# Optimization experiments

Measured on AMD Instinct MI355X. Metric: run time of the kernel, lower is better.

The kernel has to match this reference:

```python
import jax, jax.numpy as jnp
import numpy as np


def setup_inputs() -> dict:
    key = jax.random.key(0)
    kx, kd = jax.random.split(key)
    B, C, T_phone = 32, 512, 1024
    x = jax.random.normal(kx, (B, C, T_phone), dtype=jnp.float32)
    durations = jax.random.randint(kd, (B, T_phone), 0, 8, dtype=jnp.int32)
    return {"x": x, "durations": durations}


def reference(x, durations):
    # x: [B, C, T_phone] float; durations: [B, T_phone] int
    B, C, T_phone = x.shape
    cum = jnp.cumsum(durations, axis=1)            # [B, T_phone] exclusive-end frame offsets
    total = cum[:, -1]                             # [B] total frames per utterance
    max_frames = int(jnp.max(total))               # T_frame (data-dependent, computed eagerly)
    t = jnp.arange(max_frames)                     # [T_frame]
    # frame t belongs to the first phone p with cum[b, p] > t (zero-duration phones skipped)
    p = jax.vmap(lambda c: jnp.searchsorted(c, t, side="right"))(cum)  # [B, T_frame]
    valid = t[None, :] < total[:, None]            # [B, T_frame] frames inside utterance
    p = jnp.clip(p, 0, T_phone - 1)
    idx = jnp.broadcast_to(p[:, None, :], (B, C, max_frames))
    out = jnp.take_along_axis(x, idx, axis=2)      # [B, C, T_frame] gather phone features
    out = jnp.where(valid[:, None, :], out, jnp.zeros((), dtype=x.dtype))
    mel_mask = ~valid                              # True where padding (matches torch ref)
    return out, mel_mask
```

## Files before the change

kernel.cpp:

```cpp
#include <hip/hip_runtime.h>

#define B 32
#define C 512
#define TP 1024
#define CHUNK 64

__global__ void __launch_bounds__(TP) cumsum_k(const int* __restrict__ dur,
                                               int* __restrict__ cum) {
    __shared__ int s[TP];
    const int b = blockIdx.x;
    const int tid = threadIdx.x;
    s[tid] = dur[b * TP + tid];
    __syncthreads();
    for (int off = 1; off < TP; off <<= 1) {
        int v = (tid >= off) ? s[tid - off] : 0;
        __syncthreads();
        s[tid] += v;
        __syncthreads();
    }
    cum[b * TP + tid] = s[tid];
}

__global__ void __launch_bounds__(256) gather_k(const float* __restrict__ x,
                                                const int* __restrict__ cum,
                                                float* __restrict__ out,
                                                float* __restrict__ mask,
                                                int MF) {
    __shared__ int scum[TP];
    const int b = blockIdx.y;
    const int t = blockIdx.x * 256 + threadIdx.x;

    for (int i = threadIdx.x; i < TP; i += 256) scum[i] = cum[b * TP + i];
    __syncthreads();

    if (t >= MF) return;

    const int total = scum[TP - 1];
    const bool valid = (t < total);

    int lo = 0, hi = TP;
    while (lo < hi) {
        int mid = (lo + hi) >> 1;
        if (scum[mid] <= t) lo = mid + 1; else hi = mid;
    }
    int p = lo < (TP - 1) ? lo : (TP - 1);

    if (blockIdx.z == 0) {
        mask[(size_t)b * MF + t] = valid ? 0.0f : 1.0f;
    }

    const float* xb = x   + ((size_t)b * C + (size_t)blockIdx.z * CHUNK) * TP;
    float*       ob = out + ((size_t)b * C + (size_t)blockIdx.z * CHUNK) * MF;

    if (valid) {
        #pragma unroll 4
        for (int c = 0; c < CHUNK; ++c)
            ob[(size_t)c * MF + t] = xb[(size_t)c * TP + p];
    } else {
        #pragma unroll 4
        for (int c = 0; c < CHUNK; ++c)
            ob[(size_t)c * MF + t] = 0.0f;
    }
}

extern "C" void kernel_launch(void* const* d_in, const int* in_sizes, int n_in,
                              void* d_out, int out_size, void* d_ws, size_t ws_size,
                              hipStream_t stream) {
    const float* x   = (const float*)d_in[0];
    const int*   dur = (const int*)d_in[1];
    float* out = (float*)d_out;

    const int MF = out_size / (B * (C + 1));
    float* mask = out + (size_t)B * C * MF;

    int* cum = (int*)d_ws;

    cumsum_k<<<B, TP, 0, stream>>>(dur, cum);

    dim3 grid((MF + 255) / 256, B, C / CHUNK);
    gather_k<<<grid, 256, 0, stream>>>(x, cum, out, mask, MF);
}
```

Baseline: 338.7 us.

## Precompute phone indices once and gather four frames per thread

```diff
diff --git a/kernel.cpp b/kernel.cpp
--- a/kernel.cpp
+++ b/kernel.cpp
@@ -3,63 +3,84 @@
 #define B 32
 #define C 512
 #define TP 1024
-#define CHUNK 64
+#define CHUNK 32
 
-__global__ void __launch_bounds__(TP) cumsum_k(const int* __restrict__ dur,
-                                               int* __restrict__ cum) {
-    __shared__ int s[TP];
-    const int b = blockIdx.x;
-    const int tid = threadIdx.x;
-    s[tid] = dur[b * TP + tid];
+__global__ void __launch_bounds__(256) cumsum_k(const int* __restrict__ dur,
+                                                int* __restrict__ cum) {
+    const int b = blockIdx.x, tid = threadIdx.x;
+    const int lane = tid & 63, wid = tid >> 6;
+    int4 v = ((const int4*)(dur + b * TP))[tid];
+    const int s1 = v.x + v.y, s2 = s1 + v.z, s3 = s2 + v.w;
+    int val = s3;
+    #pragma unroll
+    for (int off = 1; off < 64; off <<= 1) {
+        int n = __shfl_up(val, off, 64);
+        if (lane >= off) val += n;
+    }
+    __shared__ int wtot[4];
+    if (lane == 63) wtot[wid] = val;
     __syncthreads();
-    for (int off = 1; off < TP; off <<= 1) {
-        int v = (tid >= off) ? s[tid - off] : 0;
-        __syncthreads();
-        s[tid] += v;
-        __syncthreads();
-    }
-    cum[b * TP + tid] = s[tid];
+    int base = 0;
+    #pragma unroll
+    for (int w = 0; w < 4; ++w)
+        if (w < wid) base += wtot[w];
+    const int excl = base + val - s3;
+    int4 o;
+    o.x = excl + v.x; o.y = excl + s1; o.z = excl + s2; o.w = excl + s3;
+    ((int4*)(cum + b * TP))[tid] = o;
 }
 
-__global__ void __launch_bounds__(256) gather_k(const float* __restrict__ x,
-                                                const int* __restrict__ cum,
-                                                float* __restrict__ out,
-                                                float* __restrict__ mask,
-                                                int MF) {
+__global__ void __launch_bounds__(256) phone_k(const int* __restrict__ cum,
+                                               int* __restrict__ pidx,
+                                               float* __restrict__ mask,
+                                               int MF) {
     __shared__ int scum[TP];
     const int b = blockIdx.y;
-    const int t = blockIdx.x * 256 + threadIdx.x;
-
     for (int i = threadIdx.x; i < TP; i += 256) scum[i] = cum[b * TP + i];
     __syncthreads();
-
+    const int t = blockIdx.x * 256 + threadIdx.x;
     if (t >= MF) return;
-
     const int total = scum[TP - 1];
-    const bool valid = (t < total);
-
     int lo = 0, hi = TP;
     while (lo < hi) {
         int mid = (lo + hi) >> 1;
         if (scum[mid] <= t) lo = mid + 1; else hi = mid;
     }
-    int p = lo < (TP - 1) ? lo : (TP - 1);
+    const bool valid = (t < total);
+    pidx[(size_t)b * MF + t] = valid ? (lo < TP - 1 ? lo : TP - 1) : -1;
+    mask[(size_t)b * MF + t] = valid ? 0.0f : 1.0f;
+}
 
-    if (blockIdx.z == 0) {
-        mask[(size_t)b * MF + t] = valid ? 0.0f : 1.0f;
+__global__ void __launch_bounds__(256) gather_k(const float* __restrict__ x,
+                                                const int* __restrict__ pidx,
+                                                float* __restrict__ out,
+                                                int MF) {
+    const int b = blockIdx.y, z = blockIdx.z;
+    const int tbase = blockIdx.x * 1024 + threadIdx.x;
+    const int* pb = pidx + (size_t)b * MF;
+
+    int t[4], p[4], q[4];
+    #pragma unroll
+    for (int j = 0; j < 4; ++j) {
+        t[j] = tbase + j * 256;
+        p[j] = (t[j] < MF) ? pb[t[j]] : -2;
+        q[j] = p[j] >= 0 ? p[j] : 0;
     }
 
-    const float* xb = x   + ((size_t)b * C + (size_t)blockIdx.z * CHUNK) * TP;
-    float*       ob = out + ((size_t)b * C + (size_t)blockIdx.z * CHUNK) * MF;
+    const float* xb = x   + ((size_t)b * C + (size_t)z * CHUNK) * TP;
+    float*       ob = out + ((size_t)b * C + (size_t)z * CHUNK) * MF;
 
-    if (valid) {
-        #pragma unroll 4
-        for (int c = 0; c < CHUNK; ++c)
-            ob[(size_t)c * MF + t] = xb[(size_t)c * TP + p];
-    } else {
-        #pragma unroll 4
-        for (int c = 0; c < CHUNK; ++c)
-            ob[(size_t)c * MF + t] = 0.0f;
+    #pragma unroll 2
+    for (int c = 0; c < CHUNK; ++c) {
+        const float* xr = xb + (size_t)c * TP;
+        float* orow     = ob + (size_t)c * MF;
+        #pragma unroll
+        for (int j = 0; j < 4; ++j) {
+            if (p[j] != -2) {
+                float v = xr[q[j]];
+                orow[t[j]] = (p[j] >= 0) ? v : 0.0f;
+            }
+        }
     }
 }
 
@@ -73,10 +94,14 @@
     const int MF = out_size / (B * (C + 1));
     float* mask = out + (size_t)B * C * MF;
 
-    int* cum = (int*)d_ws;
+    int* cum  = (int*)d_ws;
+    int* pidx = cum + (size_t)B * TP;
 
-    cumsum_k<<<B, TP, 0, stream>>>(dur, cum);
+    cumsum_k<<<B, 256, 0, stream>>>(dur, cum);
 
-    dim3 grid((MF + 255) / 256, B, C / CHUNK);
-    gather_k<<<grid, 256, 0, stream>>>(x, cum, out, mask, MF);
+    dim3 pgrid((MF + 255) / 256, B);
+    phone_k<<<pgrid, 256, 0, stream>>>(cum, pidx, mask, MF);
+
+    dim3 ggrid((MF + 1023) / 1024, B, C / CHUNK);
+    gather_k<<<ggrid, 256, 0, stream>>>(x, pidx, out, MF);
 }
```

Measured after the change: 374.4 us. 1.11x slower.
